# Performance work log

Measured on AMD Instinct MI355X. Metric: run time of the kernel, lower is better.

Reference implementation:

```python
import jax, jax.numpy as jnp
import numpy as np

B, S, D, H = 8, 1024, 512, 8
Dh = D // H
MASK_FILL = -1e32


def _xavier_uniform(key, shape):
    fan_in, fan_out = shape[-1], shape[-2] if len(shape) > 1 else shape[-1]
    limit = float(np.sqrt(6.0 / (fan_in + fan_out)))
    return jax.random.uniform(key, shape, jnp.float32, -limit, limit)


def setup_inputs() -> dict:
    key = jax.random.key(0)
    ks = jax.random.split(key, 8)
    q = jax.random.normal(ks[0], (B, S, D), jnp.float32)
    k = jax.random.normal(ks[1], (B, S, D), jnp.float32)
    v = jax.random.normal(ks[2], (B, S, D), jnp.float32)
    # causal mask, broadcast over batch and heads
    mask = jnp.tril(jnp.ones((S, S), dtype=bool))[None, None]
    # key_query_same=True -> one shared W for q and k
    Wq = _xavier_uniform(ks[3], (D, D)); bq = jnp.zeros((D,), jnp.float32)
    Wv = _xavier_uniform(ks[4], (D, D)); bv = jnp.zeros((D,), jnp.float32)
    Wo = _xavier_uniform(ks[5], (D, D)); bo = jnp.zeros((D,), jnp.float32)
    # gammas: (H,1,1), xavier_uniform with fan_in=fan_out=1 -> limit sqrt(3)
    lim = float(np.sqrt(3.0))
    gammas = jax.random.uniform(ks[6], (H, 1, 1), jnp.float32, -lim, lim)
    return {"q": q, "k": k, "v": v, "mask": mask,
            "Wq": Wq, "bq": bq, "Wv": Wv, "bv": bv,
            "Wo": Wo, "bo": bo, "gammas": gammas}


def reference(q, k, v, mask, Wq, bq, Wv, bv, Wo, bo, gammas):
    b, s, d = q.shape
    # projections (key_query_same -> Wq used for both q and k)
    qh = (jnp.einsum("bsd,ed->bse", q, Wq) + bq).reshape(b, s, H, Dh).transpose(0, 2, 1, 3)
    kh = (jnp.einsum("bsd,ed->bse", k, Wq) + bq).reshape(b, s, H, Dh).transpose(0, 2, 1, 3)
    vh = (jnp.einsum("bsd,ed->bse", v, Wv) + bv).reshape(b, s, H, Dh).transpose(0, 2, 1, 3)

    scale = 1.0 / jnp.sqrt(jnp.asarray(Dh, jnp.float32))
    scores = jnp.einsum("bhqd,bhkd->bhqk", qh, kh) * scale  # [B,H,S,S]

    # --- distance-decay effect (no-grad in original) ---
    pos = jnp.arange(s, dtype=jnp.float32)
    position_effect = jnp.abs(pos[None, :] - pos[:, None])[None, None]  # [1,1,S,S]
    scores_ = jax.nn.softmax(jnp.where(mask, scores, MASK_FILL), axis=-1)
    distcum = jnp.cumsum(scores_, axis=-1)
    disttotal = jnp.sum(scores_, axis=-1, keepdims=True)
    dist_scores = jnp.sqrt(jnp.clip((disttotal - distcum) * position_effect, 0.0, None))
    dist_scores = jax.lax.stop_gradient(dist_scores)

    gamma = -jnp.abs(gammas)[None]  # [1,H,1,1]
    total_effect = jnp.clip(jnp.exp(dist_scores * gamma), 1e-5, 1e5)
    scores = scores * total_effect

    scores = jax.nn.softmax(jnp.where(mask, scores, MASK_FILL), axis=-1)
    scores = jnp.where(mask, scores, 0.0)  # hard zero, avoid leakage

    v_ = jnp.einsum("bhqk,bhkd->bhqd", scores, vh)
    concat = v_.transpose(0, 2, 1, 3).reshape(b, s, d)
    output = jnp.einsum("bsd,ed->bse", concat, Wo) + bo
    return output, scores
```

## Files before the change

kernel.cpp:

```cpp
#include <hip/hip_runtime.h>
#include <hip/hip_bf16.h>

#define PB 8
#define PS 1024
#define PD 512
#define PH 8

typedef __attribute__((ext_vector_type(8))) short short8;
typedef __attribute__((ext_vector_type(4))) float f32x4;

__device__ inline ushort f2bf(float x) {
    union { float f; unsigned u; } c; c.f = x;
    unsigned u = c.u + 0x7fffu + ((c.u >> 16) & 1u);
    return (ushort)(u >> 16);
}
__device__ inline float bf2f(ushort u) {
    union { unsigned u; float f; } c; c.u = (unsigned)u << 16; return c.f;
}

__device__ inline void gload16(const void* g, void* l) {
    __builtin_amdgcn_global_load_lds(
        (const __attribute__((address_space(1))) void*)g,
        (__attribute__((address_space(3))) void*)l, 16, 0, 0);
}

__global__ __launch_bounds__(256)
void cast_all(const float* __restrict__ q, const float* __restrict__ k,
              const float* __restrict__ v, const float* __restrict__ Wq,
              const float* __restrict__ Wv, const float* __restrict__ Wo,
              ushort* __restrict__ q_bf, ushort* __restrict__ k_bf,
              ushort* __restrict__ v_bf, ushort* __restrict__ Wq_bf,
              ushort* __restrict__ Wv_bf, ushort* __restrict__ Wo_bf)
{
    const int bid = blockIdx.x;
    const float* s; ushort* d; int base;
    if      (bid < 4096)  { s = q;  d = q_bf;  base = bid; }
    else if (bid < 8192)  { s = k;  d = k_bf;  base = bid - 4096; }
    else if (bid < 12288) { s = v;  d = v_bf;  base = bid - 8192; }
    else if (bid < 12544) { s = Wq; d = Wq_bf; base = bid - 12288; }
    else if (bid < 12800) { s = Wv; d = Wv_bf; base = bid - 12544; }
    else                  { s = Wo; d = Wo_bf; base = bid - 12800; }
    const int i = base * 256 + threadIdx.x;
    const float4 x = ((const float4*)s)[i];
    ushort4 o;
    o.x = f2bf(x.x); o.y = f2bf(x.y); o.z = f2bf(x.z); o.w = f2bf(x.w);
    ((ushort4*)d)[i] = o;
}

__global__ __launch_bounds__(256)
void proj3(const ushort* __restrict__ q_bf, const ushort* __restrict__ k_bf,
           const ushort* __restrict__ v_bf, const ushort* __restrict__ Wq_bf,
           const ushort* __restrict__ Wv_bf, const float* __restrict__ bq,
           const float* __restrict__ bv, ushort* __restrict__ qh,
           ushort* __restrict__ kh, ushort* __restrict__ vhT)
{
    const int z = blockIdx.z;
    const ushort* A = (z == 0) ? q_bf : (z == 1) ? k_bf : v_bf;
    const ushort* B = (z == 2) ? Wv_bf : Wq_bf;
    const float* bias = (z == 2) ? bv : bq;

    __shared__ __align__(16) ushort As[128 * 64];
    __shared__ __align__(16) ushort Bs[128 * 64];
    const int tid = threadIdx.x;
    const int lane = tid & 63;
    const int wave = tid >> 6;
    const int wr = wave >> 1, wc = wave & 1;
    const int bm = blockIdx.x * 128, bn = blockIdx.y * 128;
    const int lrow = lane >> 3;
    const int lcol = (lane & 7) * 8;

    f32x4 acc[4][4] = {};

    for (int k0 = 0; k0 < 512; k0 += 64) {
#pragma unroll
        for (int i = 0; i < 4; ++i) {
            const int c = wave * 4 + i;
            gload16(A + (size_t)(bm + c * 8 + lrow) * 512 + k0 + lcol, &As[c * 512]);
            gload16(B + (size_t)(bn + c * 8 + lrow) * 512 + k0 + lcol, &Bs[c * 512]);
        }
        __syncthreads();
        short8 af[2][4], bf[2][4];
#pragma unroll
        for (int kk = 0; kk < 2; ++kk) {
#pragma unroll
            for (int m = 0; m < 4; ++m)
                af[kk][m] = *(const short8*)&As[(wr * 64 + m * 16 + (lane & 15)) * 64 + kk * 32 + (lane >> 4) * 8];
#pragma unroll
            for (int n = 0; n < 4; ++n)
                bf[kk][n] = *(const short8*)&Bs[(wc * 64 + n * 16 + (lane & 15)) * 64 + kk * 32 + (lane >> 4) * 8];
        }
#pragma unroll
        for (int kk = 0; kk < 2; ++kk)
#pragma unroll
            for (int m = 0; m < 4; ++m)
#pragma unroll
                for (int n = 0; n < 4; ++n)
                    acc[m][n] = __builtin_amdgcn_mfma_f32_16x16x32_bf16(af[kk][m], bf[kk][n], acc[m][n], 0, 0, 0);
        __syncthreads();
    }

#pragma unroll
    for (int m = 0; m < 4; ++m)
#pragma unroll
        for (int n = 0; n < 4; ++n) {
            const int row0 = bm + wr * 64 + m * 16 + (lane >> 4) * 4;
            const int col  = bn + wc * 64 + n * 16 + (lane & 15);
            const int b = row0 >> 10, s0 = row0 & 1023;
            const int h = col >> 6, d = col & 63;
            if (z == 2) {
                ushort4 o;
                o.x = f2bf(acc[m][n][0] + bias[col]);
                o.y = f2bf(acc[m][n][1] + bias[col]);
                o.z = f2bf(acc[m][n][2] + bias[col]);
                o.w = f2bf(acc[m][n][3] + bias[col]);
                *(ushort4*)&vhT[((size_t)((b * 8 + h) * 64 + d)) * 1024 + s0] = o;
            } else {
                ushort* out = z ? kh : qh;
#pragma unroll
                for (int r = 0; r < 4; ++r)
                    out[(((size_t)(b * 8 + h)) * 1024 + s0 + r) * 64 + d] =
                        f2bf(acc[m][n][r] + bias[col]);
            }
        }
}

__global__ __launch_bounds__(256)
void qk_mfma(const ushort* __restrict__ qh, const ushort* __restrict__ kh,
             float* __restrict__ scores)
{
    const int d0 = blockIdx.x;
    const int bh = d0 & 63;
    const int pair = d0 >> 6;
    const int kb = pair & 7, qb = pair >> 3;
    const int tid = threadIdx.x;
    if (kb > qb) {
        float* S = scores + ((size_t)bh << 20);
        const f32x4 z = {};
#pragma unroll
        for (int it = 0; it < 16; ++it) {
            const int f = it * 256 + tid;
            const int row = f >> 5, c4 = f & 31;
            __builtin_nontemporal_store(z,
                (f32x4*)&S[(size_t)(qb * 128 + row) * 1024 + kb * 128 + c4 * 4]);
        }
        return;
    }
    __shared__ __align__(16) ushort As[128 * 64];
    __shared__ __align__(16) ushort Bs[128 * 64];
    const int lane = tid & 63, wave = tid >> 6;
    const int wr = wave >> 1, wc = wave & 1;
    const ushort* Ab = qh + ((size_t)bh * PS + qb * 128) * 64;
    const ushort* Bb = kh + ((size_t)bh * PS + kb * 128) * 64;

#pragma unroll
    for (int i = 0; i < 4; ++i) {
        const int c = wave * 4 + i;
        gload16(Ab + c * 512 + lane * 8, &As[c * 512]);
        gload16(Bb + c * 512 + lane * 8, &Bs[c * 512]);
    }
    __syncthreads();

    f32x4 acc[4][4] = {};
    short8 af[2][4], bf[2][4];
#pragma unroll
    for (int kk = 0; kk < 2; ++kk) {
#pragma unroll
        for (int m = 0; m < 4; ++m)
            af[kk][m] = *(const short8*)&As[(wr * 64 + m * 16 + (lane & 15)) * 64 + kk * 32 + (lane >> 4) * 8];
#pragma unroll
        for (int n = 0; n < 4; ++n)
            bf[kk][n] = *(const short8*)&Bs[(wc * 64 + n * 16 + (lane & 15)) * 64 + kk * 32 + (lane >> 4) * 8];
    }
#pragma unroll
    for (int kk = 0; kk < 2; ++kk)
#pragma unroll
        for (int m = 0; m < 4; ++m)
#pragma unroll
            for (int n = 0; n < 4; ++n)
                acc[m][n] = __builtin_amdgcn_mfma_f32_16x16x32_bf16(af[kk][m], bf[kk][n], acc[m][n], 0, 0, 0);

    ushort* Sr = (ushort*)(scores + ((size_t)bh << 20));
#pragma unroll
    for (int m = 0; m < 4; ++m)
#pragma unroll
        for (int n = 0; n < 4; ++n)
#pragma unroll
            for (int r = 0; r < 4; ++r) {
                const int row = qb * 128 + wr * 64 + m * 16 + (lane >> 4) * 4 + r;
                const int col = kb * 128 + wc * 64 + n * 16 + (lane & 15);
                Sr[(size_t)row * 2048 + col] = f2bf(acc[m][n][r] * 0.125f);
            }
}

__global__ __launch_bounds__(1024)
void row_soft(float* __restrict__ scores, const float* __restrict__ gammas)
{
    const int d0 = blockIdx.x;
    const int bh = d0 & 63, h = bh & 7;
    const int i = (d0 >> 6) * 16 + (threadIdx.x >> 6);
    const int lane = threadIdx.x & 63;
    const int lim = ((i >> 7) + 1) * 128;
    float* srow = scores + ((size_t)bh << 20) + ((size_t)i << 10);
    const ushort* rraw = (const ushort*)srow;
    const int base = lane * 16;

    union U8 { uint4 v; ushort u[8]; };
    float l[16];
    if (base <= i) {
        U8 a, c2;
        a.v  = *(const uint4*)(rraw + base);
        c2.v = *(const uint4*)(rraw + base + 8);
#pragma unroll
        for (int c = 0; c < 8; ++c) { l[c] = bf2f(a.u[c]); l[c + 8] = bf2f(c2.u[c]); }
#pragma unroll
        for (int c = 0; c < 16; ++c) if (base + c > i) l[c] = -3.0e38f;
    } else {
#pragma unroll
        for (int c = 0; c < 16; ++c) l[c] = -3.0e38f;
    }

    float m1 = -3.0e38f;
#pragma unroll
    for (int c = 0; c < 16; ++c) m1 = fmaxf(m1, l[c]);
#pragma unroll
    for (int off = 32; off; off >>= 1) m1 = fmaxf(m1, __shfl_xor(m1, off));

    float cum[16];
    float lsum = 0.f;
#pragma unroll
    for (int c = 0; c < 16; ++c) {
        const float e = (base + c <= i) ? __expf(l[c] - m1) : 0.f;
        lsum += e;
        cum[c] = lsum;
    }
    float incl = lsum;
#pragma unroll
    for (int off = 1; off < 64; off <<= 1) {
        const float y = __shfl_up(incl, off);
        if (lane >= off) incl += y;
    }
    const float excl = incl - lsum;
    const float es = __shfl(incl, 63);
    const float inv_es = 1.0f / es;
    const float gamma = -fabsf(gammas[h]);

    float m2 = -3.0e38f;
#pragma unroll
    for (int c = 0; c < 16; ++c) {
        if (base + c <= i) {
            const float pe = (float)(i - (base + c));
            const float sfx = fmaxf((es - (excl + cum[c])) * inv_es, 0.f);
            const float dist = sqrtf(sfx * pe);
            const float eff = fmaxf(__expf(gamma * dist), 1e-5f);
            l[c] *= eff;
            m2 = fmaxf(m2, l[c]);
        }
    }
#pragma unroll
    for (int off = 32; off; off >>= 1) m2 = fmaxf(m2, __shfl_xor(m2, off));

    float s2 = 0.f;
#pragma unroll
    for (int c = 0; c < 16; ++c) {
        const float p = (base + c <= i) ? __expf(l[c] - m2) : 0.f;
        l[c] = p; s2 += p;
    }
#pragma unroll
    for (int off = 32; off; off >>= 1) s2 += __shfl_xor(s2, off);
    const float inv2 = 1.0f / s2;
#pragma unroll
    for (int c = 0; c < 16; ++c) l[c] *= inv2;

    if (base < lim) {
#pragma unroll
        for (int g = 0; g < 4; ++g) {
            f32x4 v;
            v[0] = l[g * 4 + 0]; v[1] = l[g * 4 + 1];
            v[2] = l[g * 4 + 2]; v[3] = l[g * 4 + 3];
            __builtin_nontemporal_store(v, (f32x4*)&srow[base + g * 4]);
        }
    }
}

__global__ __launch_bounds__(256)
void pv_mfma(const float* __restrict__ scores, const ushort* __restrict__ vhT,
             ushort* __restrict__ attn)
{
    const int d0 = blockIdx.x;
    const int bh = d0 & 63, qb = d0 >> 6;
    const int b = bh >> 3, h = bh & 7;
    const int lane = threadIdx.x & 63, wave = threadIdx.x >> 6;
    const int wr = wave >> 1, wc = wave & 1;
    const int lg = lane >> 4, l15 = lane & 15;
    const float* S = scores + ((size_t)bh << 20);
    const ushort* VT = vhT + ((size_t)bh << 16);
    const int nt = 2 * (qb + 1);

    const float* pa[4];
#pragma unroll
    for (int m = 0; m < 4; ++m)
        pa[m] = S + (size_t)(qb * 128 + wr * 64 + m * 16 + l15) * 1024;
    const ushort* pb[2];
#pragma unroll
    for (int n = 0; n < 2; ++n)
        pb[n] = VT + (size_t)(wc * 32 + n * 16 + l15) * 1024;

    f32x4 acc[4][2] = {};
    union U8 { short8 s; ushort u[8]; };

    for (int t = 0; t < nt; ++t) {
        const int off = t * 64 + lg * 8;
        short8 af[2][4], bf[2][2];
#pragma unroll
        for (int kk = 0; kk < 2; ++kk)
#pragma unroll
            for (int m = 0; m < 4; ++m) {
                const float4 x = *(const float4*)&pa[m][off + kk * 32];
                const float4 y = *(const float4*)&pa[m][off + kk * 32 + 4];
                U8 pk;
                pk.u[0] = f2bf(x.x); pk.u[1] = f2bf(x.y);
                pk.u[2] = f2bf(x.z); pk.u[3] = f2bf(x.w);
                pk.u[4] = f2bf(y.x); pk.u[5] = f2bf(y.y);
                pk.u[6] = f2bf(y.z); pk.u[7] = f2bf(y.w);
                af[kk][m] = pk.s;
            }
#pragma unroll
        for (int kk = 0; kk < 2; ++kk)
#pragma unroll
            for (int n = 0; n < 2; ++n)
                bf[kk][n] = *(const short8*)&pb[n][off + kk * 32];
#pragma unroll
        for (int kk = 0; kk < 2; ++kk)
#pragma unroll
            for (int m = 0; m < 4; ++m)
#pragma unroll
                for (int n = 0; n < 2; ++n)
                    acc[m][n] = __builtin_amdgcn_mfma_f32_16x16x32_bf16(af[kk][m], bf[kk][n], acc[m][n], 0, 0, 0);
    }

#pragma unroll
    for (int m = 0; m < 4; ++m)
#pragma unroll
        for (int n = 0; n < 2; ++n)
#pragma unroll
            for (int r = 0; r < 4; ++r) {
                const int row = qb * 128 + wr * 64 + m * 16 + lg * 4 + r;
                const int d = wc * 32 + n * 16 + l15;
                attn[((size_t)(b * 1024 + row)) * 512 + h * 64 + d] = f2bf(acc[m][n][r]);
            }
}

__global__ __launch_bounds__(256)
void gemm_out(const ushort* __restrict__ A, const ushort* __restrict__ B,
              const float* __restrict__ bias, float* __restrict__ out)
{
    __shared__ __align__(16) ushort As[128 * 64];
    __shared__ __align__(16) ushort Bs[128 * 64];
    const int tid = threadIdx.x;
    const int lane = tid & 63;
    const int wave = tid >> 6;
    const int wr = wave >> 1, wc = wave & 1;
    const int bm = blockIdx.x * 128, bn = blockIdx.y * 128;
    const int lrow = lane >> 3;
    const int lcol = (lane & 7) * 8;

    f32x4 acc[4][4] = {};

    for (int k0 = 0; k0 < 512; k0 += 64) {
#pragma unroll
        for (int i = 0; i < 4; ++i) {
            const int c = wave * 4 + i;
            gload16(A + (size_t)(bm + c * 8 + lrow) * 512 + k0 + lcol, &As[c * 512]);
            gload16(B + (size_t)(bn + c * 8 + lrow) * 512 + k0 + lcol, &Bs[c * 512]);
        }
        __syncthreads();
        short8 af[2][4], bf[2][4];
#pragma unroll
        for (int kk = 0; kk < 2; ++kk) {
#pragma unroll
            for (int m = 0; m < 4; ++m)
                af[kk][m] = *(const short8*)&As[(wr * 64 + m * 16 + (lane & 15)) * 64 + kk * 32 + (lane >> 4) * 8];
#pragma unroll
            for (int n = 0; n < 4; ++n)
                bf[kk][n] = *(const short8*)&Bs[(wc * 64 + n * 16 + (lane & 15)) * 64 + kk * 32 + (lane >> 4) * 8];
        }
#pragma unroll
        for (int kk = 0; kk < 2; ++kk)
#pragma unroll
            for (int m = 0; m < 4; ++m)
#pragma unroll
                for (int n = 0; n < 4; ++n)
                    acc[m][n] = __builtin_amdgcn_mfma_f32_16x16x32_bf16(af[kk][m], bf[kk][n], acc[m][n], 0, 0, 0);
        __syncthreads();
    }

#pragma unroll
    for (int m = 0; m < 4; ++m)
#pragma unroll
        for (int n = 0; n < 4; ++n)
#pragma unroll
            for (int r = 0; r < 4; ++r) {
                const int row = bm + wr * 64 + m * 16 + (lane >> 4) * 4 + r;
                const int col = bn + wc * 64 + n * 16 + (lane & 15);
                out[(size_t)row * 512 + col] = acc[m][n][r] + bias[col];
            }
}

extern "C" void kernel_launch(void* const* d_in, const int* in_sizes, int n_in,
                              void* d_out, int out_size, void* d_ws, size_t ws_size,
                              hipStream_t stream)
{
    const float* q      = (const float*)d_in[0];
    const float* k      = (const float*)d_in[1];
    const float* v      = (const float*)d_in[2];
    const float* Wq     = (const float*)d_in[4];
    const float* bq     = (const float*)d_in[5];
    const float* Wv     = (const float*)d_in[6];
    const float* bv     = (const float*)d_in[7];
    const float* Wo     = (const float*)d_in[8];
    const float* bo     = (const float*)d_in[9];
    const float* gammas = (const float*)d_in[10];

    float* out    = (float*)d_out;
    float* scores = out + (size_t)PB * PS * PD;

    char* w = (char*)d_ws;
    ushort* q_bf  = (ushort*)(w);
    ushort* k_bf  = (ushort*)(w + (8u  << 20));
    ushort* v_bf  = (ushort*)(w + (16u << 20));
    ushort* Wq_bf = (ushort*)(w + (24u << 20));
    ushort* Wv_bf = (ushort*)(w + (24u << 20) + (1u << 19));
    ushort* Wo_bf = (ushort*)(w + (25u << 20));
    ushort* qh    = (ushort*)(w + (26u << 20));
    ushort* kh    = (ushort*)(w + (34u << 20));
    ushort* vhT   = (ushort*)(w + (42u << 20));
    ushort* attn  = (ushort*)(w + (50u << 20));

    cast_all<<<13056, 256, 0, stream>>>(q, k, v, Wq, Wv, Wo,
                                        q_bf, k_bf, v_bf, Wq_bf, Wv_bf, Wo_bf);

    proj3<<<dim3(64, 4, 3), 256, 0, stream>>>(q_bf, k_bf, v_bf, Wq_bf, Wv_bf,
                                              bq, bv, qh, kh, vhT);

    qk_mfma<<<4096, 256, 0, stream>>>(qh, kh, scores);
    row_soft<<<4096, 1024, 0, stream>>>(scores, gammas);
    pv_mfma<<<512, 256, 0, stream>>>(scores, vhT, attn);

    gemm_out<<<dim3(64, 4), 256, 0, stream>>>(attn, Wo_bf, bo, out);
}
```

Before: 250.3 us.

## Fuse P@V into row softmax kernel using shared-memory bf16 probabilities

Merges the row-softmax kernel and the separate P@V MFMA kernel into one. Each 16-row block writes its normalized probabilities as bf16 into XOR-swizzled LDS. Its 16 waves then split the key range and the output columns for MFMA, and reduce partial sums through shared memory. This removes the re-read of the fp32 score matrix and a kernel launch. In exchange it adds about 49KB of LDS per block, which may limit occupancy, and each small block re-reads V from global memory.

```diff
diff --git a/kernel.cpp b/kernel.cpp
--- a/kernel.cpp
+++ b/kernel.cpp
@@ -193,13 +193,22 @@
 }
 
 __global__ __launch_bounds__(1024)
-void row_soft(float* __restrict__ scores, const float* __restrict__ gammas)
+void rowpv2(float* __restrict__ scores, const ushort* __restrict__ vhT,
+            const float* __restrict__ gammas, ushort* __restrict__ attn)
 {
     const int d0 = blockIdx.x;
     const int bh = d0 & 63, h = bh & 7;
-    const int i = (d0 >> 6) * 16 + (threadIdx.x >> 6);
+    const int b = bh >> 3;
+    const int rb = d0 >> 6;
+    const int w = threadIdx.x >> 6;
     const int lane = threadIdx.x & 63;
+    const int i = rb * 16 + w;
+    const int nt = (rb >> 2) + 1;
     const int lim = ((i >> 7) + 1) * 128;
+
+    __shared__ __align__(16) ushort P[16 * 1024];
+    __shared__ float RED[4][16][68];
+
     float* srow = scores + ((size_t)bh << 20) + ((size_t)i << 10);
     const ushort* rraw = (const ushort*)srow;
     const int base = lane * 16;
@@ -280,74 +289,40 @@
             __builtin_nontemporal_store(v, (f32x4*)&srow[base + g * 4]);
         }
     }
-}
-
-__global__ __launch_bounds__(256)
-void pv_mfma(const float* __restrict__ scores, const ushort* __restrict__ vhT,
-             ushort* __restrict__ attn)
-{
-    const int d0 = blockIdx.x;
-    const int bh = d0 & 63, qb = d0 >> 6;
-    const int b = bh >> 3, h = bh & 7;
-    const int lane = threadIdx.x & 63, wave = threadIdx.x >> 6;
-    const int wr = wave >> 1, wc = wave & 1;
-    const int lg = lane >> 4, l15 = lane & 15;
-    const float* S = scores + ((size_t)bh << 20);
-    const ushort* VT = vhT + ((size_t)bh << 16);
-    const int nt = 2 * (qb + 1);
-
-    const float* pa[4];
-#pragma unroll
-    for (int m = 0; m < 4; ++m)
-        pa[m] = S + (size_t)(qb * 128 + wr * 64 + m * 16 + l15) * 1024;
-    const ushort* pb[2];
-#pragma unroll
-    for (int n = 0; n < 2; ++n)
-        pb[n] = VT + (size_t)(wc * 32 + n * 16 + l15) * 1024;
-
-    f32x4 acc[4][2] = {};
-    union U8 { short8 s; ushort u[8]; };
-
-    for (int t = 0; t < nt; ++t) {
-        const int off = t * 64 + lg * 8;
-        short8 af[2][4], bf[2][2];
-#pragma unroll
-        for (int kk = 0; kk < 2; ++kk)
-#pragma unroll
-            for (int m = 0; m < 4; ++m) {
-                const float4 x = *(const float4*)&pa[m][off + kk * 32];
-                const float4 y = *(const float4*)&pa[m][off + kk * 32 + 4];
-                U8 pk;
-                pk.u[0] = f2bf(x.x); pk.u[1] = f2bf(x.y);
-                pk.u[2] = f2bf(x.z); pk.u[3] = f2bf(x.w);
-                pk.u[4] = f2bf(y.x); pk.u[5] = f2bf(y.y);
-                pk.u[6] = f2bf(y.z); pk.u[7] = f2bf(y.w);
-                af[kk][m] = pk.s;
-            }
-#pragma unroll
-        for (int kk = 0; kk < 2; ++kk)
-#pragma unroll
-            for (int n = 0; n < 2; ++n)
-                bf[kk][n] = *(const short8*)&pb[n][off + kk * 32];
-#pragma unroll
-        for (int kk = 0; kk < 2; ++kk)
-#pragma unroll
-            for (int m = 0; m < 4; ++m)
-#pragma unroll
-                for (int n = 0; n < 2; ++n)
-                    acc[m][n] = __builtin_amdgcn_mfma_f32_16x16x32_bf16(af[kk][m], bf[kk][n], acc[m][n], 0, 0, 0);
-    }
-
-#pragma unroll
-    for (int m = 0; m < 4; ++m)
-#pragma unroll
-        for (int n = 0; n < 2; ++n)
-#pragma unroll
-            for (int r = 0; r < 4; ++r) {
-                const int row = qb * 128 + wr * 64 + m * 16 + lg * 4 + r;
-                const int d = wc * 32 + n * 16 + l15;
-                attn[((size_t)(b * 1024 + row)) * 512 + h * 64 + d] = f2bf(acc[m][n][r]);
-            }
+
+    if (base < nt * 64) {
+        U8 p0, p1;
+#pragma unroll
+        for (int c = 0; c < 8; ++c) { p0.u[c] = f2bf(l[c]); p1.u[c] = f2bf(l[c + 8]); }
+        const int c0 = 2 * lane, c1 = 2 * lane + 1;
+        const int s0 = (c0 & ~7) | ((c0 ^ w) & 7);
+        const int s1 = (c1 & ~7) | ((c1 ^ w) & 7);
+        *(uint4*)&P[w * 1024 + s0 * 8] = p0.v;
+        *(uint4*)&P[w * 1024 + s1 * 8] = p1.v;
+    }
+    __syncthreads();
+
+    const int kq = w >> 2, nn = w & 3;
+    const int row16 = lane & 15, kg = lane >> 4;
+    const ushort* vb = vhT + ((size_t)bh << 16) + (size_t)(nn * 16 + row16) * 1024;
+    f32x4 acc = {};
+    for (int t = kq; t < nt; t += 4) {
+#pragma unroll
+        for (int kk = 0; kk < 2; ++kk) {
+            const int chunk = t * 8 + ((kk * 4 + kg) ^ (row16 & 7));
+            const short8 af = *(const short8*)&P[row16 * 1024 + chunk * 8];
+            const short8 bf = *(const short8*)&vb[t * 64 + kk * 32 + kg * 8];
+            acc = __builtin_amdgcn_mfma_f32_16x16x32_bf16(af, bf, acc, 0, 0, 0);
+        }
+    }
+
+#pragma unroll
+    for (int r = 0; r < 4; ++r)
+        RED[kq][kg * 4 + r][nn * 16 + row16] = acc[r];
+    __syncthreads();
+    const float o = RED[0][w][lane] + RED[1][w][lane] +
+                    RED[2][w][lane] + RED[3][w][lane];
+    attn[((size_t)(b * 1024 + i)) * 512 + h * 64 + lane] = f2bf(o);
 }
 
 __global__ __launch_bounds__(256)
@@ -443,8 +418,7 @@
                                               bq, bv, qh, kh, vhT);
 
     qk_mfma<<<4096, 256, 0, stream>>>(qh, kh, scores);
-    row_soft<<<4096, 1024, 0, stream>>>(scores, gammas);
-    pv_mfma<<<512, 256, 0, stream>>>(scores, vhT, attn);
+    rowpv2<<<4096, 1024, 0, stream>>>(scores, vhT, gammas, attn);
 
     gemm_out<<<dim3(64, 4), 256, 0, stream>>>(attn, Wo_bf, bo, out);
 }
```

New measurement: 242.3 us. -3.2%, faster.
